# Optimization experiments

Measured on AMD Instinct MI355X. Metric: run time of the kernel, lower is better.

## Reference

```python
import jax, jax.numpy as jnp
import numpy as np

OFFSETS = [(dx, dy, dz) for dx in (-1, 0, 1) for dy in (-1, 0, 1) for dz in (-1, 0, 1)
           if not (dx == 0 and dy == 0 and dz == 0)]  # 26 neighbor directions


def setup_inputs() -> dict:
    key = jax.random.key(0)
    k1, k2, k3, k4 = jax.random.split(key, 4)
    B, L, C_in, C_out = 2, 64, 32, 64
    x = jax.random.normal(k1, (B, L, L, L, C_in), dtype=jnp.float32)
    occupancy = (jax.random.uniform(k2, (B, L, L, L)) < 0.5).astype(jnp.float32)
    # 26 message Dense layers: kernel [2*C_in, C_out], bias [C_out]
    Wm = jax.random.normal(k3, (26, 2 * C_in, C_out), dtype=jnp.float32) / np.sqrt(2 * C_in)
    bm = jnp.zeros((26, C_out), dtype=jnp.float32)
    # update Dense: kernel [C_in + C_out, C_out]
    Wu = jax.random.normal(k4, (C_in + C_out, C_out), dtype=jnp.float32) / np.sqrt(C_in + C_out)
    bu = jnp.zeros((C_out,), dtype=jnp.float32)
    return {"x": x, "occupancy": occupancy, "Wm": Wm, "bm": bm, "Wu": Wu, "bu": bu}


def reference(x, occupancy, Wm, bm, Wu, bu):
    C_in = x.shape[-1]
    occ = occupancy[..., None]  # [B,Lx,Ly,Lz,1]
    # split each message kernel into self/neighbor halves to avoid 26 concats
    W_self = Wm[:, :C_in, :]   # [26, C_in, C_out]
    W_nb = Wm[:, C_in:, :]     # [26, C_in, C_out]
    agg = jnp.zeros(x.shape[:-1] + (Wm.shape[-1],), dtype=x.dtype)
    denom = jnp.zeros(occ.shape, dtype=x.dtype)
    for i, (dx, dy, dz) in enumerate(OFFSETS):
        x_nb = jnp.roll(x, (dx, dy, dz), axis=(1, 2, 3))
        occ_nb = jnp.roll(occ, (dx, dy, dz), axis=(1, 2, 3))
        pre = (jnp.einsum('bxyzc,cd->bxyzd', x, W_self[i])
               + jnp.einsum('bxyzc,cd->bxyzd', x_nb, W_nb[i])
               + bm[i])
        msg = jax.nn.relu(pre)
        agg = agg + msg * occ_nb
        denom = denom + occ_nb
    agg = agg / (denom + 1e-08)
    update_in = jnp.concatenate([x, agg], axis=-1)  # [B,Lx,Ly,Lz,C_in+C_out]
    out = jnp.einsum('bxyzc,cd->bxyzd', update_in, Wu) + bu
    return out * occ
```

## Files before the change

kernel.cpp:

```cpp
#include <hip/hip_runtime.h>

typedef __attribute__((ext_vector_type(8))) short bf16x8;
typedef __attribute__((ext_vector_type(4))) float f32x4;

__device__ __forceinline__ unsigned short f2bf(float f) {
  unsigned int u = __builtin_bit_cast(unsigned int, f);
  unsigned int r = (u + 0x7FFFu + ((u >> 16) & 1u)) >> 16;
  return (unsigned short)r;
}

__global__ void prep_weights(const float* __restrict__ Wm,
                             const float* __restrict__ Wu,
                             unsigned short* __restrict__ wm_img,
                             unsigned short* __restrict__ wu_img) {
  const int i = blockIdx.x;
  const int tid = threadIdx.x;
  if (i < 26) {
    for (int e = tid; e < 4096; e += 256) {
      const int col = e & 63, k = e >> 6;
      const float v = Wm[(i * 64 + k) * 64 + col];
      const int bo = col * 128 + (((k >> 3) ^ (col & 7)) << 4) + (k & 7) * 2;
      wm_img[i * 4096 + (bo >> 1)] = f2bf(v);
    }
  } else {
    for (int e = tid; e < 8192; e += 256) {
      const int col = e >> 7, k = e & 127;
      const float v = (k < 96) ? Wu[k * 64 + col] : 0.0f;
      const int bo = col * 256 + (((k >> 3) ^ (col & 7)) << 4) + (k & 7) * 2;
      wu_img[bo >> 1] = f2bf(v);
    }
  }
}

#define CB_STRIDE 10384
__global__ __launch_bounds__(512, 4)
void voxconv_main(const float* __restrict__ x,
                  const float* __restrict__ occ,
                  const float* __restrict__ bm,
                  const float* __restrict__ bu,
                  const unsigned short* __restrict__ wm_img,
                  const unsigned short* __restrict__ wu_img,
                  float* __restrict__ out) {
  __shared__ __align__(16) unsigned short x_lds[2 * CB_STRIDE];
  __shared__ __align__(16) float occ_lds[648];
  __shared__ __align__(16) unsigned short wm_buf[8192];

  const int tid  = (int)threadIdx.x;
  const int lane = tid & 63;
  const int w    = tid >> 6;
  const int q    = lane >> 4;
  const int m    = lane & 15;
  const int l7   = lane & 7;

  const int id = (int)blockIdx.x;
  const int b  = id >> 10;
  const int ix = (id >> 6) & 15;
  const int iy = (id >> 2) & 15;
  const int iz = id & 3;
  const int x0 = ix << 2, y0 = iy << 2, z0 = iz << 4;

  for (int it = 0; it < 6; ++it) {
    const int t = tid + it * 512;
    if (t < 2592) {
      const int cb = t & 3;
      const int v  = t >> 2;
      const int hz = v % 18;
      const int v2 = v / 18;
      const int hy = v2 % 6;
      const int hx = v2 / 6;
      const int X = (x0 + 63 + hx) & 63;
      const int Y = (y0 + 63 + hy) & 63;
      const int Z = (z0 + 63 + hz) & 63;
      const int vox = ((b * 64 + X) * 64 + Y) * 64 + Z;
      const float4* s4 = (const float4*)(x + vox * 32 + cb * 8);
      const float4 f0 = s4[0];
      const float4 f1 = s4[1];
      uint4 P;
      P.x = (unsigned)f2bf(f0.x) | ((unsigned)f2bf(f0.y) << 16);
      P.y = (unsigned)f2bf(f0.z) | ((unsigned)f2bf(f0.w) << 16);
      P.z = (unsigned)f2bf(f1.x) | ((unsigned)f2bf(f1.y) << 16);
      P.w = (unsigned)f2bf(f1.z) | ((unsigned)f2bf(f1.w) << 16);
      *(uint4*)((char*)x_lds + cb * CB_STRIDE + hx * 1728 + hy * 288 + hz * 16) = P;
    }
  }
  for (int t = tid; t < 648; t += 512) {
    const int hz = t % 18;
    const int v2 = t / 18;
    const int hy = v2 % 6;
    const int hx = v2 / 6;
    const int X = (x0 + 63 + hx) & 63;
    const int Y = (y0 + 63 + hy) & 63;
    const int Z = (z0 + 63 + hz) & 63;
    occ_lds[t] = occ[((b * 64 + X) * 64 + Y) * 64 + Z];
  }
  ((uint4*)wm_buf)[tid] = ((const uint4*)wm_img)[tid];
  __syncthreads();

  int aSelf[2], occSelf[2], voxBase[2];
  #pragma unroll
  for (int gg = 0; gg < 2; ++gg) {
    const int g  = w * 2 + gg;
    const int tx = g >> 2, ty = g & 3;
    aSelf[gg]   = q * CB_STRIDE + (tx + 1) * 1728 + (ty + 1) * 288 + (1 + m) * 16;
    occSelf[gg] = (tx + 1) * 108 + (ty + 1) * 18 + 1 + q * 4;
    voxBase[gg] = ((b * 64 + (x0 + tx)) * 64 + (y0 + ty)) * 64 + z0;
  }
  int bOffS[4], bOffN[4], colIdx[4];
  #pragma unroll
  for (int tt = 0; tt < 4; ++tt) {
    const int col = tt * 16 + m;
    colIdx[tt] = col;
    bOffS[tt] = col * 128 + ((q ^ l7) << 4);
    bOffN[tt] = col * 128 + (((4 + q) ^ l7) << 4);
  }

  bf16x8 aS[2];
  #pragma unroll
  for (int gg = 0; gg < 2; ++gg)
    aS[gg] = *(const bf16x8*)((const char*)x_lds + aSelf[gg]);

  float agg[2][4][4];
  float den[2][4];
  #pragma unroll
  for (int gg = 0; gg < 2; ++gg)
    #pragma unroll
    for (int j = 0; j < 4; ++j) {
      den[gg][j] = 0.0f;
      #pragma unroll
      for (int tt = 0; tt < 4; ++tt) agg[gg][tt][j] = 0.0f;
    }

  const unsigned short* gsrc_base = wm_img + 4096 + (unsigned)tid * 8;

  int cur = 0;
  #pragma unroll 1
  for (int i = 0; i < 26; ++i) {
    if (i < 25) {
      __builtin_amdgcn_global_load_lds(
          (const __attribute__((address_space(1))) void*)(gsrc_base + (unsigned)i * 4096),
          (__attribute__((address_space(3))) void*)((char*)wm_buf + (cur ^ 1) * 8192 + w * 1024 + (lane * 16)),
          16, 0, 0);
    }

    float bmv[4];
    #pragma unroll
    for (int tt = 0; tt < 4; ++tt) bmv[tt] = bm[i * 64 + colIdx[tt]];

    const int oi  = (i < 13) ? i : i + 1;
    const int dxo = oi / 9 - 1;
    const int dyo = (oi / 3) % 3 - 1;
    const int dzo = oi % 3 - 1;
    const int dA = -(dxo * 1728 + dyo * 288 + dzo * 16);
    const int dO = -(dxo * 108 + dyo * 18 + dzo);

    bf16x8 aN[2];
    float on[2][4];
    #pragma unroll
    for (int gg = 0; gg < 2; ++gg) {
      aN[gg] = *(const bf16x8*)((const char*)x_lds + aSelf[gg] + dA);
      #pragma unroll
      for (int j = 0; j < 4; ++j) on[gg][j] = occ_lds[occSelf[gg] + dO + j];
    }

    const char* wmc = (const char*)wm_buf + cur * 8192;
    #pragma unroll
    for (int tt = 0; tt < 4; ++tt) {
      const bf16x8 bS = *(const bf16x8*)(wmc + bOffS[tt]);
      const bf16x8 bN = *(const bf16x8*)(wmc + bOffN[tt]);
      #pragma unroll
      for (int gg = 0; gg < 2; ++gg) {
        f32x4 acc = {bmv[tt], bmv[tt], bmv[tt], bmv[tt]};
        acc = __builtin_amdgcn_mfma_f32_16x16x32_bf16(aS[gg], bS, acc, 0, 0, 0);
        acc = __builtin_amdgcn_mfma_f32_16x16x32_bf16(aN[gg], bN, acc, 0, 0, 0);
        #pragma unroll
        for (int j = 0; j < 4; ++j) {
          const float msg = fmaxf(acc[j], 0.0f);
          agg[gg][tt][j] = fmaf(msg, on[gg][j], agg[gg][tt][j]);
        }
      }
    }
    #pragma unroll
    for (int gg = 0; gg < 2; ++gg)
      #pragma unroll
      for (int j = 0; j < 4; ++j) den[gg][j] += on[gg][j];

    __syncthreads();
    cur ^= 1;
  }

  #pragma unroll
  for (int gg = 0; gg < 2; ++gg)
    #pragma unroll
    for (int j = 0; j < 4; ++j) {
      const float r = 1.0f / (den[gg][j] + 1e-8f);
      #pragma unroll
      for (int tt = 0; tt < 4; ++tt) agg[gg][tt][j] *= r;
    }

  char* scratch = (char*)wm_buf + w * 2048;
  float buv[4];
  #pragma unroll
  for (int tt = 0; tt < 4; ++tt) buv[tt] = bu[colIdx[tt]];

  #pragma unroll
  for (int gg = 0; gg < 2; ++gg) {
    #pragma unroll
    for (int tt = 0; tt < 4; ++tt) {
      const int colhi = tt * 2 + ((lane >> 3) & 1);
      #pragma unroll
      for (int j = 0; j < 4; ++j) {
        const int row = q * 4 + j;
        const int bo = row * 128 + ((colhi ^ (row & 7)) << 4) + l7 * 2;
        *(unsigned short*)(scratch + bo) = f2bf(agg[gg][tt][j]);
      }
    }
    const bf16x8 ag0 = *(const bf16x8*)(scratch + m * 128 + ((q ^ (m & 7)) << 4));
    const bf16x8 ag1 = *(const bf16x8*)(scratch + m * 128 + (((4 + q) ^ (m & 7)) << 4));
    float os[4];
    #pragma unroll
    for (int j = 0; j < 4; ++j) os[j] = occ_lds[occSelf[gg] + j];
    #pragma unroll
    for (int tt = 0; tt < 4; ++tt) {
      const char* wc = (const char*)wu_img + colIdx[tt] * 256;
      const bf16x8 bux  = *(const bf16x8*)(wc + ((q ^ l7) << 4));
      const bf16x8 bua0 = *(const bf16x8*)(wc + (((4 + q) ^ l7) << 4));
      const bf16x8 bua1 = *(const bf16x8*)(wc + (((8 + q) ^ l7) << 4));
      f32x4 acc = {buv[tt], buv[tt], buv[tt], buv[tt]};
      acc = __builtin_amdgcn_mfma_f32_16x16x32_bf16(aS[gg], bux,  acc, 0, 0, 0);
      acc = __builtin_amdgcn_mfma_f32_16x16x32_bf16(ag0,    bua0, acc, 0, 0, 0);
      acc = __builtin_amdgcn_mfma_f32_16x16x32_bf16(ag1,    bua1, acc, 0, 0, 0);
      #pragma unroll
      for (int j = 0; j < 4; ++j) {
        out[(voxBase[gg] + q * 4 + j) * 64 + colIdx[tt]] = acc[j] * os[j];
      }
    }
  }
}

extern "C" void kernel_launch(void* const* d_in, const int* in_sizes, int n_in,
                              void* d_out, int out_size, void* d_ws, size_t ws_size,
                              hipStream_t stream) {
  const float* x   = (const float*)d_in[0];
  const float* occ = (const float*)d_in[1];
  const float* Wm  = (const float*)d_in[2];
  const float* bm  = (const float*)d_in[3];
  const float* Wu  = (const float*)d_in[4];
  const float* bu  = (const float*)d_in[5];
  float* out = (float*)d_out;

  unsigned short* wm_img = (unsigned short*)d_ws;
  unsigned short* wu_img = wm_img + 26 * 4096;

  prep_weights<<<27, 256, 0, stream>>>(Wm, Wu, wm_img, wu_img);
  voxconv_main<<<2048, 512, 0, stream>>>(x, occ, bm, bu, wm_img, wu_img, out);
}
```

Before: 185.1 us.

## Read message weights directly from global memory instead of LDS double buffer

Drops the per-iteration async global-to-LDS double-buffered staging of the 26 message weight matrices. MFMA B operands are now loaded straight from global (L1/L2-cached) memory in a plain col-major bf16 layout without the XOR swizzle. This also removes the block-wide barrier in each of the 26 iterations. In exchange, every wave issues its own global loads for weights that were previously shared through LDS, and those loads have higher latency.

```diff
diff --git a/kernel.cpp b/kernel.cpp
--- a/kernel.cpp
+++ b/kernel.cpp
@@ -18,16 +18,12 @@
   if (i < 26) {
     for (int e = tid; e < 4096; e += 256) {
       const int col = e & 63, k = e >> 6;
-      const float v = Wm[(i * 64 + k) * 64 + col];
-      const int bo = col * 128 + (((k >> 3) ^ (col & 7)) << 4) + (k & 7) * 2;
-      wm_img[i * 4096 + (bo >> 1)] = f2bf(v);
+      wm_img[i * 4096 + col * 64 + k] = f2bf(Wm[(i * 64 + k) * 64 + col]);
     }
   } else {
     for (int e = tid; e < 8192; e += 256) {
       const int col = e >> 7, k = e & 127;
-      const float v = (k < 96) ? Wu[k * 64 + col] : 0.0f;
-      const int bo = col * 256 + (((k >> 3) ^ (col & 7)) << 4) + (k & 7) * 2;
-      wu_img[bo >> 1] = f2bf(v);
+      wu_img[col * 128 + k] = (k < 96) ? f2bf(Wu[k * 64 + col]) : (unsigned short)0;
     }
   }
 }
@@ -43,14 +39,13 @@
                   float* __restrict__ out) {
   __shared__ __align__(16) unsigned short x_lds[2 * CB_STRIDE];
   __shared__ __align__(16) float occ_lds[648];
-  __shared__ __align__(16) unsigned short wm_buf[8192];
+  __shared__ __align__(16) unsigned short sc_lds[8192];
 
   const int tid  = (int)threadIdx.x;
   const int lane = tid & 63;
   const int w    = tid >> 6;
   const int q    = lane >> 4;
   const int m    = lane & 15;
-  const int l7   = lane & 7;
 
   const int id = (int)blockIdx.x;
   const int b  = id >> 10;
@@ -93,7 +88,6 @@
     const int Z = (z0 + 63 + hz) & 63;
     occ_lds[t] = occ[((b * 64 + X) * 64 + Y) * 64 + Z];
   }
-  ((uint4*)wm_buf)[tid] = ((const uint4*)wm_img)[tid];
   __syncthreads();
 
   int aSelf[2], occSelf[2], voxBase[2];
@@ -105,13 +99,12 @@
     occSelf[gg] = (tx + 1) * 108 + (ty + 1) * 18 + 1 + q * 4;
     voxBase[gg] = ((b * 64 + (x0 + tx)) * 64 + (y0 + ty)) * 64 + z0;
   }
-  int bOffS[4], bOffN[4], colIdx[4];
+  int bOffS[4], colIdx[4];
   #pragma unroll
   for (int tt = 0; tt < 4; ++tt) {
     const int col = tt * 16 + m;
     colIdx[tt] = col;
-    bOffS[tt] = col * 128 + ((q ^ l7) << 4);
-    bOffN[tt] = col * 128 + (((4 + q) ^ l7) << 4);
+    bOffS[tt] = col * 128 + q * 16;
   }
 
   bf16x8 aS[2];
@@ -130,18 +123,8 @@
       for (int tt = 0; tt < 4; ++tt) agg[gg][tt][j] = 0.0f;
     }
 
-  const unsigned short* gsrc_base = wm_img + 4096 + (unsigned)tid * 8;
-
-  int cur = 0;
   #pragma unroll 1
   for (int i = 0; i < 26; ++i) {
-    if (i < 25) {
-      __builtin_amdgcn_global_load_lds(
-          (const __attribute__((address_space(1))) void*)(gsrc_base + (unsigned)i * 4096),
-          (__attribute__((address_space(3))) void*)((char*)wm_buf + (cur ^ 1) * 8192 + w * 1024 + (lane * 16)),
-          16, 0, 0);
-    }
-
     float bmv[4];
     #pragma unroll
     for (int tt = 0; tt < 4; ++tt) bmv[tt] = bm[i * 64 + colIdx[tt]];
@@ -162,11 +145,11 @@
       for (int j = 0; j < 4; ++j) on[gg][j] = occ_lds[occSelf[gg] + dO + j];
     }
 
-    const char* wmc = (const char*)wm_buf + cur * 8192;
+    const char* wmc = (const char*)(wm_img + i * 4096);
     #pragma unroll
     for (int tt = 0; tt < 4; ++tt) {
       const bf16x8 bS = *(const bf16x8*)(wmc + bOffS[tt]);
-      const bf16x8 bN = *(const bf16x8*)(wmc + bOffN[tt]);
+      const bf16x8 bN = *(const bf16x8*)(wmc + bOffS[tt] + 64);
       #pragma unroll
       for (int gg = 0; gg < 2; ++gg) {
         f32x4 acc = {bmv[tt], bmv[tt], bmv[tt], bmv[tt]};
@@ -183,9 +166,6 @@
     for (int gg = 0; gg < 2; ++gg)
       #pragma unroll
       for (int j = 0; j < 4; ++j) den[gg][j] += on[gg][j];
-
-    __syncthreads();
-    cur ^= 1;
   }
 
   #pragma unroll
@@ -197,7 +177,8 @@
       for (int tt = 0; tt < 4; ++tt) agg[gg][tt][j] *= r;
     }
 
-  char* scratch = (char*)wm_buf + w * 2048;
+  char* scratch = (char*)sc_lds + w * 2048;
+  const int l7 = lane & 7;
   float buv[4];
   #pragma unroll
   for (int tt = 0; tt < 4; ++tt) buv[tt] = bu[colIdx[tt]];
@@ -221,10 +202,10 @@
     for (int j = 0; j < 4; ++j) os[j] = occ_lds[occSelf[gg] + j];
     #pragma unroll
     for (int tt = 0; tt < 4; ++tt) {
-      const char* wc = (const char*)wu_img + colIdx[tt] * 256;
-      const bf16x8 bux  = *(const bf16x8*)(wc + ((q ^ l7) << 4));
-      const bf16x8 bua0 = *(const bf16x8*)(wc + (((4 + q) ^ l7) << 4));
-      const bf16x8 bua1 = *(const bf16x8*)(wc + (((8 + q) ^ l7) << 4));
+      const char* wc = (const char*)(wu_img + colIdx[tt] * 128);
+      const bf16x8 bux  = *(const bf16x8*)(wc + q * 16);
+      const bf16x8 bua0 = *(const bf16x8*)(wc + 64 + q * 16);
+      const bf16x8 bua1 = *(const bf16x8*)(wc + 128 + q * 16);
       f32x4 acc = {buv[tt], buv[tt], buv[tt], buv[tt]};
       acc = __builtin_amdgcn_mfma_f32_16x16x32_bf16(aS[gg], bux,  acc, 0, 0, 0);
       acc = __builtin_amdgcn_mfma_f32_16x16x32_bf16(ag0,    bua0, acc, 0, 0, 0);
```

After: 453.5 us. 145% more time.
